# Kernel tuning notes

Hardware: AMD Instinct MI355X
Metric: run time of the kernel (lower is better)

The kernel has to match this reference:

```python
import jax, jax.numpy as jnp
import numpy as np


def conv1x1(x, w, b):
    # x: (B, C_in, D, H, W), w: (C_out, C_in), b: (C_out,)  -- 1x1x1 Conv3d == per-voxel linear
    return jnp.einsum('bcdhw,oc->bodhw', x, w) + b[None, :, None, None, None]


def setup_inputs() -> dict:
    key = jax.random.key(0)
    ks = jax.random.split(key, 6)
    B, C, D, H, W = 2, 64, 8, 64, 64
    K = 4096  # codebook_size after halving
    return {
        'z': jax.random.normal(ks[0], (B, C, D, H, W), dtype=jnp.float32),
        'embedding': jax.random.normal(ks[1], (K, C), dtype=jnp.float32),
        'pre_w': jax.random.normal(ks[2], (C, C), dtype=jnp.float32) * (1.0 / np.sqrt(C)),
        'pre_b': jax.random.normal(ks[3], (C,), dtype=jnp.float32) * 0.01,
        'post_w': jax.random.normal(ks[4], (C, C), dtype=jnp.float32) * (1.0 / np.sqrt(C)),
        'post_b': jax.random.normal(ks[5], (C,), dtype=jnp.float32) * 0.01,
    }


def reference(z, embedding, pre_w, pre_b, post_w, post_b):
    B, C, D, H, W = z.shape
    x = conv1x1(z, pre_w, pre_b)  # pre_quant_conv

    # ---- quantize() ----
    # tokens: (B*D*H*W, C)
    t = jnp.transpose(x, (0, 2, 3, 4, 1)).reshape(-1, C)
    # squared euclidean distances (argmin identical to torch.cdist argmin)
    dist2 = (jnp.sum(t * t, axis=-1, keepdims=True)
             - 2.0 * t @ embedding.T
             + jnp.sum(embedding * embedding, axis=-1)[None, :])  # (N, K)
    idx = jnp.argmin(dist2, axis=-1)  # (N,)
    q = embedding[idx]  # gather: (N, C)

    commitment_loss = jnp.mean((jax.lax.stop_gradient(q) - t) ** 2)
    codebook_loss = jnp.mean((q - jax.lax.stop_gradient(t)) ** 2)

    # straight-through estimator
    q = t + jax.lax.stop_gradient(q - t)
    quant = jnp.transpose(q.reshape(B, D, H, W, C), (0, 4, 1, 2, 3))

    out = conv1x1(quant, post_w, post_b)  # post_quant_conv
    indices = idx.reshape(B, D, H, W)
    return out, codebook_loss, commitment_loss, indices
```

## Files before the change

kernel.cpp:

```cpp
#include <hip/hip_runtime.h>
#include <cstdint>
#include <cstddef>

typedef float  f32x4  __attribute__((ext_vector_type(4)));
typedef float  f32x16 __attribute__((ext_vector_type(16)));
typedef short  s16x8  __attribute__((ext_vector_type(8)));

#define DEV __device__ __forceinline__

static constexpr int    DHW       = 32768;
static constexpr int    NTOK      = 65536;
static constexpr int    CHUNK_B   = 18432;
static constexpr size_t OUT_ELEMS = 4194304;
static constexpr float  BIGC      = 512.0f;
static constexpr float  TAU       = 0.015f;
static constexpr int    FLAG_CAP  = 7424;

static constexpr size_t WS_PREP = 0;
static constexpr size_t WS_RESW = 1179648;
static constexpr size_t WS_RESB = 2228224;
static constexpr size_t WS_PART = 2490368;
static constexpr size_t WS_CNT  = 2494464;
static constexpr size_t WS_FLAG = 2494720;

DEV unsigned f2bf(float f) {
  unsigned u = __float_as_uint(f);
  return (u + 0x7FFFu + ((u >> 16) & 1u)) >> 16;
}
DEV float bf2f(unsigned h) { return __uint_as_float(h << 16); }
DEV unsigned med3u(unsigned a, unsigned b, unsigned c) {
  unsigned r;
  asm("v_med3_u32 %0, %1, %2, %3" : "=v"(r) : "v"(a), "v"(b), "v"(c));
  return r;
}
DEV void gl_lds16(const void* g, void* l) {
  __builtin_amdgcn_global_load_lds(
      (const __attribute__((address_space(1))) unsigned int*)g,
      (__attribute__((address_space(3))) unsigned int*)l, 16, 0, 0);
}

__global__ __launch_bounds__(256) void k_pre(const float* __restrict__ z,
    const float* __restrict__ emb, const float* __restrict__ pw, const float* __restrict__ pb,
    float* __restrict__ dout, char* __restrict__ ws)
{
  const int blk = blockIdx.x, tid = threadIdx.x;
  if (blk == 0 && tid == 0) *(int*)(ws + WS_CNT) = 0;
  if (blk < 256) {
    float* t = dout;
    const int v = blk * 256 + tid;
    const int b = v >> 15, r = v & (DHW - 1);
    const float* zp = z + (size_t)b * 64 * DHW + r;
    float zr[64];
#pragma unroll
    for (int c2 = 0; c2 < 64; ++c2) zr[c2] = zp[(size_t)c2 * DHW];
    for (int c = 0; c < 64; c += 4) {
      const float* w0 = pw + c * 64;
      const float* w1 = pw + (c + 1) * 64;
      const float* w2 = pw + (c + 2) * 64;
      const float* w3 = pw + (c + 3) * 64;
      float a0 = pb[c], a1 = pb[c + 1], a2 = pb[c + 2], a3 = pb[c + 3];
#pragma unroll
      for (int c2 = 0; c2 < 64; ++c2) {
        const float zv = zr[c2];
        a0 = fmaf(w0[c2], zv, a0); a1 = fmaf(w1[c2], zv, a1);
        a2 = fmaf(w2[c2], zv, a2); a3 = fmaf(w3[c2], zv, a3);
      }
      t[(size_t)c * NTOK + v]       = a0;
      t[(size_t)(c + 1) * NTOK + v] = a1;
      t[(size_t)(c + 2) * NTOK + v] = a2;
      t[(size_t)(c + 3) * NTOK + v] = a3;
    }
  } else {
    const int tt = (blk - 256) * 256 + tid;
#pragma unroll
    for (int uu = 0; uu < 2; ++uu) {
      const int u = tt * 2 + uu;
      const int k = u >> 3, j = u & 7;
      const float* ep = emb + (size_t)k * 64 + j * 8;
      unsigned hw[4], lw[4];
#pragma unroll
      for (int i = 0; i < 4; ++i) {
        float g0 = -2.0f * ep[2 * i], g1 = -2.0f * ep[2 * i + 1];
        unsigned h0 = f2bf(g0); unsigned l0 = f2bf(g0 - bf2f(h0));
        unsigned h1 = f2bf(g1); unsigned l1 = f2bf(g1 - bf2f(h1));
        hw[i] = h0 | (h1 << 16); lw[i] = l0 | (l1 << 16);
      }
      char* base = ws + WS_PREP + (size_t)(k >> 6) * CHUNK_B;
      const int r = k & 63;
      const int swz = (r & 15) << 4;
      char* rowp = base + r * 256;
      *(uint4*)(rowp + ((j * 16) ^ swz))        = make_uint4(hw[0], hw[1], hw[2], hw[3]);
      *(uint4*)(rowp + ((128 + j * 16) ^ swz))  = make_uint4(lw[0], lw[1], lw[2], lw[3]);
      if (j == 0) {
        const float* er = emb + (size_t)k * 64;
        float s = 0.f;
#pragma unroll
        for (int c = 0; c < 64; ++c) s = fmaf(er[c], er[c], s);
        s += BIGC;
        unsigned eh  = f2bf(s);
        float    rs  = s - bf2f(eh);
        unsigned el  = f2bf(rs);
        unsigned el2 = f2bf(rs - bf2f(el));
        *(uint4*)(base + 16384 + r * 16) = make_uint4(eh | (el << 16), el2, 0u, 0u);
        if (r == 0) *(uint4*)(base + 16384 + 1024) = make_uint4(0u, 0u, 0u, 0u);
      }
    }
  }
}

__global__ __launch_bounds__(512, 4) void k_dist(float* __restrict__ dout,
                                                 char* __restrict__ ws)
{
  constexpr int NCH = 32;
  __shared__ __align__(16) char smem[3 * CHUNK_B];
  const float* t = dout;
  const int tid = threadIdx.x;
  const int w = tid >> 6, lane = tid & 63;
  const int l31 = lane & 31, khalf = lane >> 5;
  const int gidx = blockIdx.x >> 1, h = blockIdx.x & 1;
  const int tb = gidx * 256 + w * 32;
  const int tok = tb + l31;

  s16x8 tav[4], tlv[4];
#pragma unroll
  for (int kt = 0; kt < 4; ++kt) {
    const float* tc = t + (size_t)(kt * 16 + khalf * 8) * NTOK + tok;
    float f[8];
#pragma unroll
    for (int i = 0; i < 8; ++i) f[i] = tc[(size_t)i * NTOK];
    union { unsigned u[4]; s16x8 v; } xh, xl;
#pragma unroll
    for (int i = 0; i < 4; ++i) {
      unsigned h0 = f2bf(f[2 * i]),     l0 = f2bf(f[2 * i]     - bf2f(h0));
      unsigned h1 = f2bf(f[2 * i + 1]), l1 = f2bf(f[2 * i + 1] - bf2f(h1));
      xh.u[i] = h0 | (h1 << 16); xl.u[i] = l0 | (l1 << 16);
    }
    tav[kt] = xh.v; tlv[kt] = xl.v;
  }
  s16x8 ones;
  { union { unsigned u[4]; s16x8 v; } o;
    o.u[0] = khalf ? 0u : 0x3F803F80u;
    o.u[1] = khalf ? 0u : 0x00003F80u;
    o.u[2] = 0u; o.u[3] = 0u; ones = o.v; }

  const char* prep = ws + WS_PREP + (size_t)h * NCH * CHUNK_B;
  const int swz = (l31 & 15) << 4;

  auto stage = [&](int cc) {
    const char* src = prep + (size_t)cc * CHUNK_B;
    char* dst = smem + (size_t)(cc % 3) * CHUNK_B;
    gl_lds16(src + w * 1024 + lane * 16, dst + w * 1024);
    gl_lds16(src + 8192 + w * 1024 + lane * 16, dst + 8192 + w * 1024);
    if (w < 2) gl_lds16(src + 16384 + w * 1024 + lane * 16, dst + 16384 + w * 1024);
  };
  stage(0); stage(1);

  unsigned u1 = 0x7f800000u, u2 = 0x7f800000u;
  int c1 = 0;

  for (int c = 0; c < NCH; ++c) {
    if (c == NCH - 1)  asm volatile("s_waitcnt vmcnt(0)" ::: "memory");
    else if (w < 2)    asm volatile("s_waitcnt vmcnt(3)" ::: "memory");
    else               asm volatile("s_waitcnt vmcnt(2)" ::: "memory");
    __builtin_amdgcn_s_barrier();
    __builtin_amdgcn_sched_barrier(0);
    if (c + 2 < NCH) stage(c + 2);
    const char* L = smem + (size_t)(c % 3) * CHUNK_B;

    __builtin_amdgcn_s_setprio(1);
    f32x16 acc0 = {}, acc1 = {};
    {
      const s16x8 e0 = *(const s16x8*)(L + (khalf ? (16384 + 1024) : (16384 + l31 * 16)));
      const s16x8 e1 = *(const s16x8*)(L + (khalf ? (16384 + 1024) : (16384 + (32 + l31) * 16)));
      acc0 = __builtin_amdgcn_mfma_f32_32x32x16_bf16(e0, ones, acc0, 0, 0, 0);
      acc1 = __builtin_amdgcn_mfma_f32_32x32x16_bf16(e1, ones, acc1, 0, 0, 0);
    }
#pragma unroll
    for (int kt = 0; kt < 4; ++kt) {
      const int i0 = (kt * 32 + khalf * 16) ^ swz;
      const s16x8 gh0 = *(const s16x8*)(L + l31 * 256 + i0);
      const s16x8 gl0 = *(const s16x8*)(L + l31 * 256 + (i0 ^ 128));
      const s16x8 gh1 = *(const s16x8*)(L + (32 + l31) * 256 + i0);
      const s16x8 gl1 = *(const s16x8*)(L + (32 + l31) * 256 + (i0 ^ 128));
      acc0 = __builtin_amdgcn_mfma_f32_32x32x16_bf16(gh0, tav[kt], acc0, 0, 0, 0);
      acc0 = __builtin_amdgcn_mfma_f32_32x32x16_bf16(gh0, tlv[kt], acc0, 0, 0, 0);
      acc0 = __builtin_amdgcn_mfma_f32_32x32x16_bf16(gl0, tav[kt], acc0, 0, 0, 0);
      acc1 = __builtin_amdgcn_mfma_f32_32x32x16_bf16(gh1, tav[kt], acc1, 0, 0, 0);
      acc1 = __builtin_amdgcn_mfma_f32_32x32x16_bf16(gh1, tlv[kt], acc1, 0, 0, 0);
      acc1 = __builtin_amdgcn_mfma_f32_32x32x16_bf16(gl1, tav[kt], acc1, 0, 0, 0);
    }
    __builtin_amdgcn_s_setprio(0);
    const unsigned p1 = u1;
#pragma unroll
    for (int q = 0; q < 16; ++q) {
      const unsigned w0 = (unsigned)((q & 3) + 8 * (q >> 2));
      unsigned v0 = (__float_as_uint(acc0[q]) & ~63u) | w0;
      u2 = med3u(u1, v0, u2); u1 = u1 < v0 ? u1 : v0;
      unsigned v1 = (__float_as_uint(acc1[q]) & ~63u) | (w0 + 32u);
      u2 = med3u(u1, v1, u2); u1 = u1 < v1 ? u1 : v1;
    }
    if (u1 != p1) c1 = c;
  }

  u1 |= (unsigned)(khalf * 4);
  const unsigned o1 = __shfl_xor(u1, 32);
  const unsigned o2 = __shfl_xor(u2, 32);
  const int      oc = __shfl_xor(c1, 32);
  const unsigned am = u1 & ~63u, om = o1 & ~63u;
  const int mycode = c1 * 64 + (int)(u1 & 63u);
  const int ocode  = oc * 64 + (int)(o1 & 63u);
  const bool owins = (om < am) || (om == am && ocode < mycode);
  const unsigned f1 = owins ? o1 : u1;
  const int      fc = owins ? oc : c1;
  const unsigned mx = owins ? am : om;
  unsigned s2 = (u2 & ~63u) < (o2 & ~63u) ? (u2 & ~63u) : (o2 & ~63u);
  s2 = s2 < mx ? s2 : mx;
  if (khalf == 0) {
    const bool nt = (__uint_as_float(s2) - __uint_as_float(f1 & ~63u)) < TAU;
    ((unsigned*)(ws + WS_RESW))[h * 65536 + tok] = f1;
    ((unsigned char*)(ws + WS_RESB))[h * 65536 + tok] =
        (unsigned char)(fc | (nt ? 0x80 : 0));
  }
}

__global__ __launch_bounds__(256) void k_merge(const float* __restrict__ emb,
    float* __restrict__ dout, char* __restrict__ ws)
{
  __shared__ float ls[4];
  const int tid = threadIdx.x;
  const int v = blockIdx.x * 64 + (tid >> 2);
  const int q4 = tid & 3;
  const unsigned* resw = (const unsigned*)(ws + WS_RESW);
  const unsigned char* resb = (const unsigned char*)(ws + WS_RESB);
  const unsigned A = resw[v], B = resw[65536 + v];
  const unsigned am = A & ~63u, bm = B & ~63u;
  const bool bwins = bm < am;
  const unsigned bw = bwins ? B : A;
  const int bq = bwins ? 1 : 0;
  const unsigned k1 = bwins ? bm : am;
  const unsigned k2 = bwins ? am : bm;
  const unsigned char bb = resb[bq * 65536 + v];
  const int code = bq * 2048 + (int)(bb & 31u) * 64 + (int)(bw & 63u);
  const float* tcol = dout + v;
  const float* qe = emb + (size_t)code * 64 + q4 * 16;
  float acc = 0.f;
#pragma unroll
  for (int i = 0; i < 4; ++i) {
    const float4 qv = *(const float4*)(qe + i * 4);
#pragma unroll
    for (int j = 0; j < 4; ++j) {
      const int ch = q4 * 16 + i * 4 + j;
      const float d = tcol[(size_t)ch * NTOK] - ((const float*)&qv)[j];
      acc = fmaf(d, d, acc);
    }
  }
  acc += __shfl_xor(acc, 1);
  acc += __shfl_xor(acc, 2);
  if (q4 == 0) {
    dout[OUT_ELEMS + 2 + v] = (float)code;
    const bool flag = (bb & 0x80u) ||
                      (__uint_as_float(k2) - __uint_as_float(k1) < TAU);
    if (flag) {
      int p = atomicAdd((int*)(ws + WS_CNT), 1);
      if (p < FLAG_CAP) ((int*)(ws + WS_FLAG))[p] = v;
    }
  }
#pragma unroll
  for (int m = 4; m < 64; m <<= 1) acc += __shfl_xor(acc, m);
  const int lane = tid & 63, wv = tid >> 6;
  if (lane == 0) ls[wv] = acc;
  __syncthreads();
  if (tid == 0)
    ((float*)(ws + WS_PART))[blockIdx.x] = ls[0] + ls[1] + ls[2] + ls[3];
}

__global__ __launch_bounds__(256) void k_refine(const float* __restrict__ z,
    const float* __restrict__ emb, const float* __restrict__ pw, const float* __restrict__ pb,
    float* __restrict__ dout, char* __restrict__ ws)
{
  __shared__ double tdsh[64];
  __shared__ double dred[4]; __shared__ int kred[4];
  int cv = *(const int*)(ws + WS_CNT);
  if (cv > FLAG_CAP) cv = FLAG_CAP;
  const int slot = blockIdx.x;
  if (slot >= cv) return;
  const int tid = threadIdx.x;
  const int lane = tid & 63, wv = tid >> 6;
  const int n = ((const int*)(ws + WS_FLAG))[slot];

  if (tid < 64) {
    const int b = n >> 15, r = n & (DHW - 1);
    const float* zp = z + (size_t)b * 64 * DHW + r;
    const float* wr = pw + tid * 64;
    double a = (double)pb[tid];
    for (int c2 = 0; c2 < 64; ++c2)
      a = fma((double)wr[c2], (double)zp[(size_t)c2 * DHW], a);
    tdsh[tid] = a;
  }
  __syncthreads();

  double td[64];
#pragma unroll
  for (int j = 0; j < 64; ++j) td[j] = tdsh[j];

  double dmin = 1e300; int kmin = 0;
  for (int it = 0; it < 16; ++it) {
    const int code = it * 256 + tid;
    const float4* e = (const float4*)(emb + (size_t)code * 64);
    double d0 = 0.0, d1 = 0.0;
#pragma unroll
    for (int i = 0; i < 16; ++i) {
      const float4 ev = e[i];
      const double x0 = td[4 * i]     - (double)ev.x; d0 = fma(x0, x0, d0);
      const double x1 = td[4 * i + 1] - (double)ev.y; d1 = fma(x1, x1, d1);
      const double x2 = td[4 * i + 2] - (double)ev.z; d0 = fma(x2, x2, d0);
      const double x3 = td[4 * i + 3] - (double)ev.w; d1 = fma(x3, x3, d1);
    }
    const double d = d0 + d1;
    if (d < dmin) { dmin = d; kmin = code; }
  }
#pragma unroll
  for (int m = 1; m < 64; m <<= 1) {
    const double od = __shfl_xor(dmin, m);
    const int    ok = __shfl_xor(kmin, m);
    if (od < dmin || (od == dmin && ok < kmin)) { dmin = od; kmin = ok; }
  }
  if (lane == 0) { dred[wv] = dmin; kred[wv] = kmin; }
  __syncthreads();
  if (tid == 0) {
#pragma unroll
    for (int i = 1; i < 4; ++i)
      if (dred[i] < dmin || (dred[i] == dmin && kred[i] < kmin)) { dmin = dred[i]; kmin = kred[i]; }
    dout[OUT_ELEMS + 2 + n] = (float)kmin;
  }
}

__global__ __launch_bounds__(256) void k_post(const float* __restrict__ emb,
    const float* __restrict__ ow, const float* __restrict__ ob,
    float* __restrict__ dout, const char* __restrict__ ws)
{
  __shared__ float ps[256];
  const int v = blockIdx.x * 256 + threadIdx.x;
  const int b = v >> 15, r = v & (DHW - 1);
  const int code = (int)dout[OUT_ELEMS + 2 + v];
  const float* q = emb + (size_t)code * 64;
  float qr[64];
#pragma unroll
  for (int i = 0; i < 16; ++i) *(float4*)(qr + i * 4) = *(const float4*)(q + i * 4);
  float* op = dout + (size_t)b * 64 * DHW + r;
  for (int o = 0; o < 64; o += 4) {
    const float* w0 = ow + o * 64;
    const float* w1 = ow + (o + 1) * 64;
    const float* w2 = ow + (o + 2) * 64;
    const float* w3 = ow + (o + 3) * 64;
    float a0 = ob[o], a1 = ob[o + 1], a2 = ob[o + 2], a3 = ob[o + 3];
#pragma unroll
    for (int cch = 0; cch < 64; ++cch) {
      const float qv = qr[cch];
      a0 = fmaf(w0[cch], qv, a0); a1 = fmaf(w1[cch], qv, a1);
      a2 = fmaf(w2[cch], qv, a2); a3 = fmaf(w3[cch], qv, a3);
    }
    op[(size_t)o * DHW]       = a0;
    op[(size_t)(o + 1) * DHW] = a1;
    op[(size_t)(o + 2) * DHW] = a2;
    op[(size_t)(o + 3) * DHW] = a3;
  }
  if (blockIdx.x == 0) {
    const float* part = (const float*)(ws + WS_PART);
    const int t4 = threadIdx.x * 4;
    float s = ((part[t4] + part[t4 + 1]) + part[t4 + 2]) + part[t4 + 3];
    ps[threadIdx.x] = s;
    __syncthreads();
    if (threadIdx.x == 0) {
      float tot = 0.f;
      for (int i = 0; i < 256; ++i) tot += ps[i];
      const float mean = tot / 4194304.0f;
      dout[OUT_ELEMS]     = mean;
      dout[OUT_ELEMS + 1] = mean;
    }
  }
}

extern "C" void kernel_launch(void* const* d_in, const int* in_sizes, int n_in,
                              void* d_out, int out_size, void* d_ws, size_t ws_size,
                              hipStream_t stream) {
  (void)in_sizes; (void)n_in; (void)out_size; (void)ws_size;
  const float* z   = (const float*)d_in[0];
  const float* emb = (const float*)d_in[1];
  const float* pw  = (const float*)d_in[2];
  const float* pb  = (const float*)d_in[3];
  const float* ow  = (const float*)d_in[4];
  const float* ob  = (const float*)d_in[5];
  float* out = (float*)d_out;
  char*  ws  = (char*)d_ws;

  hipLaunchKernelGGL(k_pre,    dim3(320),  dim3(256), 0, stream, z, emb, pw, pb, out, ws);
  hipLaunchKernelGGL(k_dist,   dim3(512),  dim3(512), 0, stream, out, ws);
  hipLaunchKernelGGL(k_merge,  dim3(1024), dim3(256), 0, stream, emb, out, ws);
  hipLaunchKernelGGL(k_refine, dim3(FLAG_CAP), dim3(256), 0, stream, z, emb, pw, pb, out, ws);
  hipLaunchKernelGGL(k_post,   dim3(256),  dim3(256), 0, stream, emb, ow, ob, out, ws);
}
```

Measured before the change: 195.4 us.

## Software-pipeline MFMA distance chunks with argmin of previous chunk

Restructures the codebook chunk loop into a two-stage software pipeline: the MFMA distance computation for chunk c is issued before the argmin/top-2 reduction of chunk c-1, using double-buffered accumulators. This lets the VALU min/med3 work overlap with the matrix unit instead of serializing after each chunk's MFMAs. The cost is an extra 32 accumulator registers, which may reduce occupancy, and the s_setprio hints are dropped. It also assumes NCH is even.

```diff
diff --git a/kernel.cpp b/kernel.cpp
--- a/kernel.cpp
+++ b/kernel.cpp
@@ -153,27 +153,21 @@
     gl_lds16(src + 8192 + w * 1024 + lane * 16, dst + 8192 + w * 1024);
     if (w < 2) gl_lds16(src + 16384 + w * 1024 + lane * 16, dst + 16384 + w * 1024);
   };
-  stage(0); stage(1);
-
-  unsigned u1 = 0x7f800000u, u2 = 0x7f800000u;
-  int c1 = 0;
-
-  for (int c = 0; c < NCH; ++c) {
+  auto waitb = [&](int c) {
     if (c == NCH - 1)  asm volatile("s_waitcnt vmcnt(0)" ::: "memory");
     else if (w < 2)    asm volatile("s_waitcnt vmcnt(3)" ::: "memory");
     else               asm volatile("s_waitcnt vmcnt(2)" ::: "memory");
     __builtin_amdgcn_s_barrier();
     __builtin_amdgcn_sched_barrier(0);
-    if (c + 2 < NCH) stage(c + 2);
+  };
+  auto domfma = [&](int c, f32x16& A0, f32x16& A1) {
     const char* L = smem + (size_t)(c % 3) * CHUNK_B;
-
-    __builtin_amdgcn_s_setprio(1);
-    f32x16 acc0 = {}, acc1 = {};
+    A0 = {}; A1 = {};
     {
       const s16x8 e0 = *(const s16x8*)(L + (khalf ? (16384 + 1024) : (16384 + l31 * 16)));
       const s16x8 e1 = *(const s16x8*)(L + (khalf ? (16384 + 1024) : (16384 + (32 + l31) * 16)));
-      acc0 = __builtin_amdgcn_mfma_f32_32x32x16_bf16(e0, ones, acc0, 0, 0, 0);
-      acc1 = __builtin_amdgcn_mfma_f32_32x32x16_bf16(e1, ones, acc1, 0, 0, 0);
+      A0 = __builtin_amdgcn_mfma_f32_32x32x16_bf16(e0, ones, A0, 0, 0, 0);
+      A1 = __builtin_amdgcn_mfma_f32_32x32x16_bf16(e1, ones, A1, 0, 0, 0);
     }
 #pragma unroll
     for (int kt = 0; kt < 4; ++kt) {
@@ -182,25 +176,46 @@
       const s16x8 gl0 = *(const s16x8*)(L + l31 * 256 + (i0 ^ 128));
       const s16x8 gh1 = *(const s16x8*)(L + (32 + l31) * 256 + i0);
       const s16x8 gl1 = *(const s16x8*)(L + (32 + l31) * 256 + (i0 ^ 128));
-      acc0 = __builtin_amdgcn_mfma_f32_32x32x16_bf16(gh0, tav[kt], acc0, 0, 0, 0);
-      acc0 = __builtin_amdgcn_mfma_f32_32x32x16_bf16(gh0, tlv[kt], acc0, 0, 0, 0);
-      acc0 = __builtin_amdgcn_mfma_f32_32x32x16_bf16(gl0, tav[kt], acc0, 0, 0, 0);
-      acc1 = __builtin_amdgcn_mfma_f32_32x32x16_bf16(gh1, tav[kt], acc1, 0, 0, 0);
-      acc1 = __builtin_amdgcn_mfma_f32_32x32x16_bf16(gh1, tlv[kt], acc1, 0, 0, 0);
-      acc1 = __builtin_amdgcn_mfma_f32_32x32x16_bf16(gl1, tav[kt], acc1, 0, 0, 0);
-    }
-    __builtin_amdgcn_s_setprio(0);
+      A0 = __builtin_amdgcn_mfma_f32_32x32x16_bf16(gh0, tav[kt], A0, 0, 0, 0);
+      A0 = __builtin_amdgcn_mfma_f32_32x32x16_bf16(gh0, tlv[kt], A0, 0, 0, 0);
+      A0 = __builtin_amdgcn_mfma_f32_32x32x16_bf16(gl0, tav[kt], A0, 0, 0, 0);
+      A1 = __builtin_amdgcn_mfma_f32_32x32x16_bf16(gh1, tav[kt], A1, 0, 0, 0);
+      A1 = __builtin_amdgcn_mfma_f32_32x32x16_bf16(gh1, tlv[kt], A1, 0, 0, 0);
+      A1 = __builtin_amdgcn_mfma_f32_32x32x16_bf16(gl1, tav[kt], A1, 0, 0, 0);
+    }
+  };
+
+  unsigned u1 = 0x7f800000u, u2 = 0x7f800000u;
+  int c1 = 0;
+  auto argmin = [&](const f32x16& A0, const f32x16& A1, int CC) {
     const unsigned p1 = u1;
 #pragma unroll
     for (int q = 0; q < 16; ++q) {
       const unsigned w0 = (unsigned)((q & 3) + 8 * (q >> 2));
-      unsigned v0 = (__float_as_uint(acc0[q]) & ~63u) | w0;
+      unsigned v0 = (__float_as_uint(A0[q]) & ~63u) | w0;
       u2 = med3u(u1, v0, u2); u1 = u1 < v0 ? u1 : v0;
-      unsigned v1 = (__float_as_uint(acc1[q]) & ~63u) | (w0 + 32u);
+      unsigned v1 = (__float_as_uint(A1[q]) & ~63u) | (w0 + 32u);
       u2 = med3u(u1, v1, u2); u1 = u1 < v1 ? u1 : v1;
     }
-    if (u1 != p1) c1 = c;
-  }
+    if (u1 != p1) c1 = CC;
+  };
+
+  f32x16 a0A, a1A, a0B, a1B;
+  stage(0); stage(1);
+  waitb(0); stage(2); domfma(0, a0A, a1A);
+  waitb(1); stage(3); domfma(1, a0B, a1B); argmin(a0A, a1A, 0);
+  for (int i = 1; i < NCH / 2; ++i) {
+    const int cA = 2 * i;
+    waitb(cA);
+    if (cA + 2 < NCH) stage(cA + 2);
+    domfma(cA, a0A, a1A);
+    argmin(a0B, a1B, cA - 1);
+    waitb(cA + 1);
+    if (cA + 3 < NCH) stage(cA + 3);
+    domfma(cA + 1, a0B, a1B);
+    argmin(a0A, a1A, cA);
+  }
+  argmin(a0B, a1B, NCH - 1);
 
   u1 |= (unsigned)(khalf * 4);
   const unsigned o1 = __shfl_xor(u1, 32);
```

After: 199.7 us. 1.02x slower.
